# Kernel optimization log

Measured on AMD Instinct MI355X. Metric: run time of the kernel, lower is better.

The kernel has to match this reference:

```python
import jax, jax.numpy as jnp
import numpy as np

B, T, C, H = 4, 2048, 1024, 16
D = C // H  # head_dim = 64


def setup_inputs() -> dict:
    key = jax.random.key(0)
    ks = jax.random.split(key, 5)
    scale = 0.02
    return {
        "x": jax.random.normal(ks[0], (B, T, C), dtype=jnp.float32),
        "w_qkv": jax.random.normal(ks[1], (C, 3 * C), dtype=jnp.float32) * scale,
        "b_qkv": jnp.zeros((3 * C,), dtype=jnp.float32),
        "w_out": jax.random.normal(ks[2], (C, C), dtype=jnp.float32) * scale,
        "b_out": jnp.zeros((C,), dtype=jnp.float32),
    }


def reference(x, w_qkv, b_qkv, w_out, b_out):
    Bx, Tx, Cx = x.shape
    qkv = x @ w_qkv + b_qkv  # [B,T,3C]
    q, k, v = jnp.split(qkv, 3, axis=-1)
    # [B,T,C] -> [B,H,T,D]
    def heads(t):
        return t.reshape(Bx, Tx, H, D).transpose(0, 2, 1, 3)
    q, k, v = heads(q), heads(k), heads(v)
    scores = jnp.einsum("bhtd,bhsd->bhts", q, k) / jnp.sqrt(jnp.float32(D))
    causal = jnp.tril(jnp.ones((Tx, Tx), dtype=bool))
    scores = jnp.where(causal[None, None], scores, -jnp.inf)
    attn = jax.nn.softmax(scores, axis=-1)
    y = jnp.einsum("bhts,bhsd->bhtd", attn, v)  # [B,H,T,D]
    y = y.transpose(0, 2, 1, 3).reshape(Bx, Tx, Cx)
    return y @ w_out + b_out
```

## Files before the change

### kernel.cpp

```cpp
#include <hip/hip_runtime.h>
#include <hip/hip_bf16.h>
#include <math.h>

typedef __bf16 bf16;
typedef __bf16 bf16x8 __attribute__((ext_vector_type(8)));
typedef __bf16 bf16x4 __attribute__((ext_vector_type(4)));
typedef float  f32x4  __attribute__((ext_vector_type(4)));

__device__ __forceinline__ void gld_lds16(const bf16* g, bf16* l) {
    void* gv = (void*)g;
    __builtin_amdgcn_global_load_lds(
        (__attribute__((address_space(1))) void*)gv,
        (__attribute__((address_space(3))) void*)l, 16, 0, 0);
}

__global__ void k_cvt_bf16(const float* __restrict__ in, bf16* __restrict__ out, int n4) {
    int i = blockIdx.x * blockDim.x + threadIdx.x;
    if (i < n4) {
        float4 v = ((const float4*)in)[i];
        bf16x4 o;
        o[0] = (bf16)v.x; o[1] = (bf16)v.y; o[2] = (bf16)v.z; o[3] = (bf16)v.w;
        ((bf16x4*)out)[i] = o;
    }
}

__global__ void k_transpose_cvt(const float* __restrict__ in, bf16* __restrict__ out,
                                int R, int C) {
    __shared__ float tile[64][68];
    int c0 = blockIdx.x * 64, r0 = blockIdx.y * 64;
    int tid = threadIdx.x;
#pragma unroll
    for (int i = 0; i < 4; ++i) {
        int chunk = tid + i * 256;
        int r = chunk >> 4, c4 = (chunk & 15) * 4;
        float4 v = *(const float4*)(in + (size_t)(r0 + r) * C + c0 + c4);
        tile[r][c4 + 0] = v.x; tile[r][c4 + 1] = v.y;
        tile[r][c4 + 2] = v.z; tile[r][c4 + 3] = v.w;
    }
    __syncthreads();
#pragma unroll
    for (int i = 0; i < 2; ++i) {
        int chunk = tid + i * 256;
        int c = chunk >> 3, k8 = (chunk & 7) * 8;
        bf16x8 v;
#pragma unroll
        for (int j = 0; j < 8; ++j) v[j] = (bf16)tile[k8 + j][c];
        *(bf16x8*)(out + (size_t)(c0 + c) * R + r0 + k8) = v;
    }
}

__global__ void k_transpose_v(const bf16* __restrict__ qkv, bf16* __restrict__ vt) {
    __shared__ bf16 tile[64][72];
    int bh = blockIdx.y, b = bh >> 4, h = bh & 15;
    int t0 = blockIdx.x * 64;
    int tid = threadIdx.x;
    const bf16* src = qkv + (size_t)(b * 2048 + t0) * 3072 + 2048 + h * 64;
#pragma unroll
    for (int i = 0; i < 2; ++i) {
        int chunk = tid + i * 256;
        int t = chunk >> 3, d8 = (chunk & 7) * 8;
        bf16x8 v = *(const bf16x8*)(src + (size_t)t * 3072 + d8);
#pragma unroll
        for (int j = 0; j < 8; ++j) tile[t][d8 + j] = v[j];
    }
    __syncthreads();
#pragma unroll
    for (int i = 0; i < 2; ++i) {
        int chunk = tid + i * 256;
        int d = chunk >> 3, t8 = (chunk & 7) * 8;
        bf16x8 v;
#pragma unroll
        for (int j = 0; j < 8; ++j) v[j] = tile[t8 + j][d];
        *(bf16x8*)(vt + ((size_t)bh * 64 + d) * 2048 + t0 + t8) = v;
    }
}

template <bool OUT_BF16>
__global__ __launch_bounds__(256, 2) void k_gemm(
    const bf16* __restrict__ A, const bf16* __restrict__ Bt,
    const float* __restrict__ bias, void* __restrict__ Cout,
    int M, int N, int K) {
    __shared__ __align__(16) bf16 lA[2][4096];
    __shared__ __align__(16) bf16 lB[2][4096];
    int tid = threadIdx.x;
    int wid = tid >> 6, lane = tid & 63;
    int quad = lane >> 4, l16 = lane & 15;
    int bm = blockIdx.y * 128, bn = blockIdx.x * 128;
    int wm = (wid >> 1) * 64, wn = (wid & 1) * 64;

    f32x4 zero = {0.f, 0.f, 0.f, 0.f};
    f32x4 acc[4][4];
#pragma unroll
    for (int i = 0; i < 4; ++i)
#pragma unroll
        for (int j = 0; j < 4; ++j) acc[i][j] = zero;

    for (int k0 = 0; k0 < K; k0 += 64) {
        __syncthreads();
#pragma unroll
        for (int i = 0; i < 4; ++i) {
            int j = (wid * 4 + i) * 64 + lane;
            int kf = j >> 9, row = (j & 511) >> 2, c8 = (j & 3) * 8;
            gld_lds16(A  + (size_t)(bm + row) * K + k0 + kf * 32 + c8, &lA[0][0] + (wid * 4 + i) * 512);
            gld_lds16(Bt + (size_t)(bn + row) * K + k0 + kf * 32 + c8, &lB[0][0] + (wid * 4 + i) * 512);
        }
        __syncthreads();
#pragma unroll
        for (int kk = 0; kk < 2; ++kk) {
            bf16x8 af[4], bg[4];
#pragma unroll
            for (int i = 0; i < 4; ++i) {
                af[i] = *(const bf16x8*)(&lA[kk][(wm + i * 16 + l16) * 32 + quad * 8]);
                bg[i] = *(const bf16x8*)(&lB[kk][(wn + i * 16 + l16) * 32 + quad * 8]);
            }
#pragma unroll
            for (int i = 0; i < 4; ++i)
#pragma unroll
                for (int j = 0; j < 4; ++j)
                    acc[i][j] = __builtin_amdgcn_mfma_f32_16x16x32_bf16(af[i], bg[j], acc[i][j], 0, 0, 0);
        }
    }
#pragma unroll
    for (int i = 0; i < 4; ++i) {
#pragma unroll
        for (int j = 0; j < 4; ++j) {
            int col = bn + wn + j * 16 + l16;
            float bv = bias ? bias[col] : 0.f;
#pragma unroll
            for (int r = 0; r < 4; ++r) {
                int row = bm + wm + i * 16 + quad * 4 + r;
                float v = acc[i][j][r] + bv;
                if (OUT_BF16) ((bf16*)Cout)[(size_t)row * N + col] = (bf16)v;
                else          ((float*)Cout)[(size_t)row * N + col] = v;
            }
        }
    }
}

__global__ __launch_bounds__(256, 4) void k_attn(
    const bf16* __restrict__ qkv,
    const bf16* __restrict__ vt,
    bf16* __restrict__ y) {
    __shared__ __align__(16) bf16 lK[2][4096];
    __shared__ __align__(16) bf16 lV[4096];
    __shared__ __align__(16) bf16 lP[4][32 * 36];

    const int T = 2048, CQ = 3072;
    int tid = threadIdx.x, wid = tid >> 6, lane = tid & 63;
    int quad = lane >> 4, l16 = lane & 15;
    int x = blockIdx.x;
    int bh = ((x & 7) << 3) | ((x >> 3) & 7);
    int qb = 15 - (x >> 6);
    int b = bh >> 4, h = bh & 15;
    int q0 = qb * 128;
    int rb = qb * 4 + wid;
    int mdiag = rb >> 1;
    int ntiles = qb * 2 + 2;

    const bf16* qbase = qkv + (size_t)(b * T + q0 + wid * 32) * CQ + h * 64;
    const bf16* kbase = qkv + (size_t)(b * T) * CQ + 1024 + h * 64;
    const bf16* vbase = vt + (size_t)bh * 64 * T;
    bf16* lPw = lP[wid];

    auto stageK = [&](int kt, int buf) {
        int t0 = kt * 64;
#pragma unroll
        for (int i = 0; i < 2; ++i) {
            int j = (wid * 2 + i) * 64 + lane;
            int r = j >> 3;
            int cs = ((j ^ r) & 7) * 8;
            gld_lds16(kbase + (size_t)(t0 + r) * CQ + cs, &lK[buf][(wid * 2 + i) * 512]);
        }
    };
    auto stageV = [&](int kt) {
        int t0 = kt * 64;
#pragma unroll
        for (int i = 0; i < 2; ++i) {
            int j = (wid * 2 + i) * 64 + lane;
            int r = j >> 3;
            int cs = ((j ^ r) & 7) * 8;
            gld_lds16(vbase + (size_t)r * T + t0 + cs, &lV[(wid * 2 + i) * 512]);
        }
    };

    const float QSCALE = 0.125f * 1.44269504088896341f;
    bf16x8 qf[2][2];
#pragma unroll
    for (int qi = 0; qi < 2; ++qi)
#pragma unroll
        for (int kf = 0; kf < 2; ++kf) {
            bf16x8 v = *(const bf16x8*)(qbase + (size_t)(qi * 16 + l16) * CQ + kf * 32 + quad * 8);
#pragma unroll
            for (int j = 0; j < 8; ++j) v[j] = (bf16)((float)v[j] * QSCALE);
            qf[qi][kf] = v;
        }

    f32x4 zero = {0.f, 0.f, 0.f, 0.f};
    f32x4 minit = {-14.4269504089f, -14.4269504089f, -14.4269504089f, -14.4269504089f};
    f32x4 o[2][4];
    f32x4 ls[2];
#pragma unroll
    for (int qi = 0; qi < 2; ++qi) {
        ls[qi] = zero;
#pragma unroll
        for (int i = 0; i < 4; ++i) o[qi][i] = zero;
    }
    bf16x8 ones;
#pragma unroll
    for (int j = 0; j < 8; ++j) ones[j] = (bf16)1.0f;

    stageK(0, 0);
    for (int kt = 0; kt < ntiles; ++kt) {
        __syncthreads();
        stageV(kt);
        int knext = (kt + 1 < ntiles) ? kt + 1 : kt;
        stageK(knext, (kt + 1) & 1);
        if (kt > mdiag) continue;
        const bf16* Kb = lK[kt & 1];
        bool diag = (kt == mdiag);
        bool half = diag && !(rb & 1);
        int in_hi = half ? 2 : 4;

        f32x4 s[2][4];
#pragma unroll
        for (int in = 0; in < 4; ++in) {
            if (in >= in_hi) break;
            bf16x8 kb0 = *(const bf16x8*)(Kb + (in * 16 + l16) * 64 + ((quad ^ (l16 & 7)) * 8));
            bf16x8 kb1 = *(const bf16x8*)(Kb + (in * 16 + l16) * 64 + (((4 + quad) ^ (l16 & 7)) * 8));
#pragma unroll
            for (int qi = 0; qi < 2; ++qi) {
                f32x4 t0 = __builtin_amdgcn_mfma_f32_16x16x32_bf16(kb0, qf[qi][0], minit, 0, 0, 0);
                s[qi][in] = __builtin_amdgcn_mfma_f32_16x16x32_bf16(kb1, qf[qi][1], t0, 0, 0, 0);
            }
        }

        int rl0 = (rb * 32) - kt * 64;
#pragma unroll
        for (int kf = 0; kf < 2; ++kf) {
#pragma unroll
            for (int qi = 0; qi < 2; ++qi) {
                int qloc = rl0 + qi * 16 + l16;
#pragma unroll
                for (int in2 = 0; in2 < 2; ++in2) {
                    int in = kf * 2 + in2;
                    bf16x4 pk4;
                    if (in >= in_hi) {
                        pk4[0] = pk4[1] = pk4[2] = pk4[3] = (bf16)0.f;
                    } else {
#pragma unroll
                        for (int r = 0; r < 4; ++r) {
                            float e = __builtin_amdgcn_exp2f(s[qi][in][r]);
                            if (diag) {
                                int tloc = kf * 32 + in2 * 16 + quad * 4 + r;
                                if (tloc > qloc) e = 0.f;
                            }
                            pk4[r] = (bf16)e;
                        }
                    }
                    *(bf16x4*)(lPw + (qi * 16 + l16) * 36 + in2 * 16 + quad * 4) = pk4;
                }
            }
            if (kf == 0)
                asm volatile("s_waitcnt vmcnt(2)" ::: "memory");
            bf16x8 vb[4];
#pragma unroll
            for (int dn = 0; dn < 4; ++dn)
                vb[dn] = *(const bf16x8*)(lV + (dn * 16 + l16) * 64 + (((kf * 4 + quad) ^ (l16 & 7)) * 8));
#pragma unroll
            for (int qi = 0; qi < 2; ++qi) {
                bf16x8 pa = *(const bf16x8*)(lPw + (qi * 16 + l16) * 36 + quad * 8);
                ls[qi] = __builtin_amdgcn_mfma_f32_16x16x32_bf16(pa, ones, ls[qi], 0, 0, 0);
#pragma unroll
                for (int dn = 0; dn < 4; ++dn)
                    o[qi][dn] = __builtin_amdgcn_mfma_f32_16x16x32_bf16(pa, vb[dn], o[qi][dn], 0, 0, 0);
            }
        }
    }

#pragma unroll
    for (int qi = 0; qi < 2; ++qi)
#pragma unroll
        for (int r = 0; r < 4; ++r) {
            float li = 1.f / ls[qi][r];
            int row = q0 + wid * 32 + qi * 16 + quad * 4 + r;
#pragma unroll
            for (int dn = 0; dn < 4; ++dn) {
                float v = o[qi][dn][r] * li;
                y[(size_t)(b * T + row) * 1024 + h * 64 + dn * 16 + l16] = (bf16)v;
            }
        }
}

extern "C" void kernel_launch(void* const* d_in, const int* in_sizes, int n_in,
                              void* d_out, int out_size, void* d_ws, size_t ws_size,
                              hipStream_t stream) {
    const float* x     = (const float*)d_in[0];
    const float* w_qkv = (const float*)d_in[1];
    const float* b_qkv = (const float*)d_in[2];
    const float* w_out = (const float*)d_in[3];
    const float* b_out = (const float*)d_in[4];
    float* out = (float*)d_out;

    const int B = 4, T = 2048, C = 1024, H = 16;
    const int M = B * T;

    char* ws = (char*)d_ws;
    bf16* xb    = (bf16*)(ws);
    bf16* wqkvT = (bf16*)(ws + (16ull << 20));
    bf16* woutT = (bf16*)(ws + (22ull << 20));
    bf16* qkvb  = (bf16*)(ws + (24ull << 20));
    bf16* yb    = (bf16*)(ws + (72ull << 20));
    bf16* vtb   = xb;

    k_cvt_bf16<<<(M * C / 4 + 255) / 256, 256, 0, stream>>>(x, xb, M * C / 4);
    k_transpose_cvt<<<dim3(3 * C / 64, C / 64), 256, 0, stream>>>(w_qkv, wqkvT, C, 3 * C);
    k_transpose_cvt<<<dim3(C / 64, C / 64), 256, 0, stream>>>(w_out, woutT, C, C);
    k_gemm<true><<<dim3(3 * C / 128, M / 128), 256, 0, stream>>>(xb, wqkvT, b_qkv, qkvb, M, 3 * C, C);
    k_transpose_v<<<dim3(T / 64, B * H), 256, 0, stream>>>(qkvb, vtb);
    k_attn<<<dim3(1024, 1), 256, 0, stream>>>(qkvb, vtb, yb);
    k_gemm<false><<<dim3(C / 128, M / 128), 256, 0, stream>>>(yb, woutT, b_out, out, M, C, C);
}
```

Measured before the change: 267.8 us.

## Load V fragments directly from global into registers instead of LDS staging

Removes the shared V tile and its async global-to-LDS staging. Each wave now reads its V^T MFMA operands straight from global memory into registers. On half-masked diagonal tiles it skips the second k-half entirely, and it no longer issues a redundant K prefetch on the last tile. This cuts LDS traffic and footprint, but every wave now reloads the same V data from global/L2 instead of sharing it, and those loads are exposed latency with no prefetch ahead of use.

Measured after the change: 335.3 us. 1.25x slower.

```diff
diff --git a/kernel.cpp b/kernel.cpp
--- a/kernel.cpp
+++ b/kernel.cpp
@@ -142,7 +142,6 @@
     const bf16* __restrict__ vt,
     bf16* __restrict__ y) {
     __shared__ __align__(16) bf16 lK[2][4096];
-    __shared__ __align__(16) bf16 lV[4096];
     __shared__ __align__(16) bf16 lP[4][32 * 36];
 
     const int T = 2048, CQ = 3072;
@@ -159,7 +158,7 @@
 
     const bf16* qbase = qkv + (size_t)(b * T + q0 + wid * 32) * CQ + h * 64;
     const bf16* kbase = qkv + (size_t)(b * T) * CQ + 1024 + h * 64;
-    const bf16* vbase = vt + (size_t)bh * 64 * T;
+    const bf16* vlane = vt + ((size_t)(bh * 64 + l16)) * T + quad * 8;
     bf16* lPw = lP[wid];
 
     auto stageK = [&](int kt, int buf) {
@@ -172,16 +171,6 @@
             gld_lds16(kbase + (size_t)(t0 + r) * CQ + cs, &lK[buf][(wid * 2 + i) * 512]);
         }
     };
-    auto stageV = [&](int kt) {
-        int t0 = kt * 64;
-#pragma unroll
-        for (int i = 0; i < 2; ++i) {
-            int j = (wid * 2 + i) * 64 + lane;
-            int r = j >> 3;
-            int cs = ((j ^ r) & 7) * 8;
-            gld_lds16(vbase + (size_t)r * T + t0 + cs, &lV[(wid * 2 + i) * 512]);
-        }
-    };
 
     const float QSCALE = 0.125f * 1.44269504088896341f;
     bf16x8 qf[2][2];
@@ -212,14 +201,14 @@
     stageK(0, 0);
     for (int kt = 0; kt < ntiles; ++kt) {
         __syncthreads();
-        stageV(kt);
-        int knext = (kt + 1 < ntiles) ? kt + 1 : kt;
-        stageK(knext, (kt + 1) & 1);
+        if (kt + 1 < ntiles) stageK(kt + 1, (kt + 1) & 1);
         if (kt > mdiag) continue;
         const bf16* Kb = lK[kt & 1];
+        const bf16* Vt = vlane + kt * 64;
         bool diag = (kt == mdiag);
         bool half = diag && !(rb & 1);
         int in_hi = half ? 2 : 4;
+        int khi = half ? 1 : 2;
 
         f32x4 s[2][4];
 #pragma unroll
@@ -234,9 +223,13 @@
             }
         }
 
+        bf16x8 vb0[4], vb1[4];
+#pragma unroll
+        for (int dn = 0; dn < 4; ++dn)
+            vb0[dn] = *(const bf16x8*)(Vt + (size_t)(dn * 16) * T);
+
         int rl0 = (rb * 32) - kt * 64;
-#pragma unroll
-        for (int kf = 0; kf < 2; ++kf) {
+        for (int kf = 0; kf < khi; ++kf) {
 #pragma unroll
             for (int qi = 0; qi < 2; ++qi) {
                 int qloc = rl0 + qi * 16 + l16;
@@ -260,19 +253,19 @@
                     *(bf16x4*)(lPw + (qi * 16 + l16) * 36 + in2 * 16 + quad * 4) = pk4;
                 }
             }
-            if (kf == 0)
-                asm volatile("s_waitcnt vmcnt(2)" ::: "memory");
-            bf16x8 vb[4];
-#pragma unroll
-            for (int dn = 0; dn < 4; ++dn)
-                vb[dn] = *(const bf16x8*)(lV + (dn * 16 + l16) * 64 + (((kf * 4 + quad) ^ (l16 & 7)) * 8));
+            if (kf == 0 && khi == 2) {
+#pragma unroll
+                for (int dn = 0; dn < 4; ++dn)
+                    vb1[dn] = *(const bf16x8*)(Vt + (size_t)(dn * 16) * T + 32);
+            }
 #pragma unroll
             for (int qi = 0; qi < 2; ++qi) {
                 bf16x8 pa = *(const bf16x8*)(lPw + (qi * 16 + l16) * 36 + quad * 8);
                 ls[qi] = __builtin_amdgcn_mfma_f32_16x16x32_bf16(pa, ones, ls[qi], 0, 0, 0);
 #pragma unroll
                 for (int dn = 0; dn < 4; ++dn)
-                    o[qi][dn] = __builtin_amdgcn_mfma_f32_16x16x32_bf16(pa, vb[dn], o[qi][dn], 0, 0, 0);
+                    o[qi][dn] = __builtin_amdgcn_mfma_f32_16x16x32_bf16(
+                        pa, kf ? vb1[dn] : vb0[dn], o[qi][dn], 0, 0, 0);
             }
         }
     }
```

## Double-buffer V tiles, swizzle P scratch, skip masked half on diagonal

Applied to the files above, without the earlier changes.

V staging now uses two LDS buffers and is prefetched one tile ahead together with K, so the explicit vmcnt wait inside the PV loop goes away. The P scratch drops its 36-element padded stride for a 32-element XOR-swizzled layout to avoid bank conflicts without padding. On half-masked diagonal tiles the PV loop now runs only the first k-fragment instead of multiplying zeros. LDS use rises by one V buffer, which may lower occupancy, and the k-fragment loop is no longer unrolled.

Result: faster. 258.5 us (-3.5%).

```diff
diff --git a/kernel.cpp b/kernel.cpp
--- a/kernel.cpp
+++ b/kernel.cpp
@@ -142,8 +142,8 @@
     const bf16* __restrict__ vt,
     bf16* __restrict__ y) {
     __shared__ __align__(16) bf16 lK[2][4096];
-    __shared__ __align__(16) bf16 lV[4096];
-    __shared__ __align__(16) bf16 lP[4][32 * 36];
+    __shared__ __align__(16) bf16 lV[2][4096];
+    __shared__ __align__(16) bf16 lP[4][1024];
 
     const int T = 2048, CQ = 3072;
     int tid = threadIdx.x, wid = tid >> 6, lane = tid & 63;
@@ -161,6 +161,7 @@
     const bf16* kbase = qkv + (size_t)(b * T) * CQ + 1024 + h * 64;
     const bf16* vbase = vt + (size_t)bh * 64 * T;
     bf16* lPw = lP[wid];
+    int sE = ((l16 >> 1) & 3) * 8;
 
     auto stageK = [&](int kt, int buf) {
         int t0 = kt * 64;
@@ -172,14 +173,14 @@
             gld_lds16(kbase + (size_t)(t0 + r) * CQ + cs, &lK[buf][(wid * 2 + i) * 512]);
         }
     };
-    auto stageV = [&](int kt) {
+    auto stageV = [&](int kt, int buf) {
         int t0 = kt * 64;
 #pragma unroll
         for (int i = 0; i < 2; ++i) {
             int j = (wid * 2 + i) * 64 + lane;
             int r = j >> 3;
             int cs = ((j ^ r) & 7) * 8;
-            gld_lds16(vbase + (size_t)r * T + t0 + cs, &lV[(wid * 2 + i) * 512]);
+            gld_lds16(vbase + (size_t)r * T + t0 + cs, &lV[buf][(wid * 2 + i) * 512]);
         }
     };
 
@@ -210,16 +211,20 @@
     for (int j = 0; j < 8; ++j) ones[j] = (bf16)1.0f;
 
     stageK(0, 0);
+    stageV(0, 0);
     for (int kt = 0; kt < ntiles; ++kt) {
         __syncthreads();
-        stageV(kt);
-        int knext = (kt + 1 < ntiles) ? kt + 1 : kt;
-        stageK(knext, (kt + 1) & 1);
+        if (kt + 1 < ntiles) {
+            stageV(kt + 1, (kt + 1) & 1);
+            stageK(kt + 1, (kt + 1) & 1);
+        }
         if (kt > mdiag) continue;
         const bf16* Kb = lK[kt & 1];
+        const bf16* Vb = lV[kt & 1];
         bool diag = (kt == mdiag);
         bool half = diag && !(rb & 1);
         int in_hi = half ? 2 : 4;
+        int khi = half ? 1 : 2;
 
         f32x4 s[2][4];
 #pragma unroll
@@ -235,8 +240,7 @@
         }
 
         int rl0 = (rb * 32) - kt * 64;
-#pragma unroll
-        for (int kf = 0; kf < 2; ++kf) {
+        for (int kf = 0; kf < khi; ++kf) {
 #pragma unroll
             for (int qi = 0; qi < 2; ++qi) {
                 int qloc = rl0 + qi * 16 + l16;
@@ -257,18 +261,16 @@
                             pk4[r] = (bf16)e;
                         }
                     }
-                    *(bf16x4*)(lPw + (qi * 16 + l16) * 36 + in2 * 16 + quad * 4) = pk4;
+                    *(bf16x4*)(lPw + (qi * 16 + l16) * 32 + ((in2 * 16 + quad * 4) ^ sE)) = pk4;
                 }
             }
-            if (kf == 0)
-                asm volatile("s_waitcnt vmcnt(2)" ::: "memory");
             bf16x8 vb[4];
 #pragma unroll
             for (int dn = 0; dn < 4; ++dn)
-                vb[dn] = *(const bf16x8*)(lV + (dn * 16 + l16) * 64 + (((kf * 4 + quad) ^ (l16 & 7)) * 8));
+                vb[dn] = *(const bf16x8*)(Vb + (dn * 16 + l16) * 64 + (((kf * 4 + quad) ^ (l16 & 7)) * 8));
 #pragma unroll
             for (int qi = 0; qi < 2; ++qi) {
-                bf16x8 pa = *(const bf16x8*)(lPw + (qi * 16 + l16) * 36 + quad * 8);
+                bf16x8 pa = *(const bf16x8*)(lPw + (qi * 16 + l16) * 32 + ((quad * 8) ^ sE));
                 ls[qi] = __builtin_amdgcn_mfma_f32_16x16x32_bf16(pa, ones, ls[qi], 0, 0, 0);
 #pragma unroll
                 for (int dn = 0; dn < 4; ++dn)
```
